# Performance work log

Measured on AMD Instinct MI355X. Metric: run time of the kernel, lower is better.

## Reference

```python
import jax, jax.numpy as jnp
import numpy as np

B, S, D, H = 2, 4096, 512, 8


def setup_inputs() -> dict:
    key = jax.random.key(0)
    ks = jax.random.split(key, 8)
    sc = 1.0 / np.sqrt(D)
    return {
        "query": jax.random.normal(ks[0], (B, S, D), jnp.float32),
        "key_in": jax.random.normal(ks[1], (B, S, D), jnp.float32),
        "value": jax.random.normal(ks[2], (B, S, D), jnp.float32),
        "mask": jax.random.randint(ks[3], (B, S), 0, 2, jnp.int32),
        "Wq": jax.random.normal(ks[4], (D, D), jnp.float32) * sc,
        "bq": jnp.zeros((D,), jnp.float32),
        "Wk": jax.random.normal(ks[5], (D, D), jnp.float32) * sc,
        "bk": jnp.zeros((D,), jnp.float32),
        "Wv": jax.random.normal(ks[6], (D, D), jnp.float32) * sc,
        "bv": jnp.zeros((D,), jnp.float32),
        "Wo": jax.random.normal(ks[7], (D, D), jnp.float32) * sc,
        "bo": jnp.zeros((D,), jnp.float32),
    }


def reference(query, key_in, value, mask, Wq, bq, Wk, bk, Wv, bv, Wo, bo):
    b, s, d = query.shape
    dh = d // H  # per-head dim = out_size // attn_heads
    # projections + split heads: [B,S,D] -> [B,H,S,dh]
    q = (query @ Wq + bq).reshape(b, s, H, dh).transpose(0, 2, 1, 3)
    k = (key_in @ Wk + bk).reshape(b, s, H, dh).transpose(0, 2, 1, 3)
    v = (value @ Wv + bv).reshape(b, s, H, dh).transpose(0, 2, 1, 3)
    # scores / sqrt(dh); torch divides by sqrt(query.size(-1)) AFTER head split
    scores = jnp.einsum("bhqd,bhkd->bhqk", q, k) / jnp.sqrt(jnp.asarray(dh, q.dtype))
    # 2D mask broadcast: mask[:,None,None,:] == unsqueeze(1).repeat(1,S,1).unsqueeze(1)
    scores = jnp.where(mask[:, None, None, :] == 0, jnp.asarray(-1e9, scores.dtype), scores)
    p_attn = jax.nn.softmax(scores, axis=-1)  # dropout p=0.0 -> identity
    x = jnp.einsum("bhqk,bhkd->bhqd", p_attn, v)
    x = x.transpose(0, 2, 1, 3).reshape(b, s, H * dh)
    return x @ Wo + bo
```

## Files before the change

### kernel.cpp

```cpp
#include <hip/hip_runtime.h>
#include <math.h>

#define BATCH  2
#define SLEN   4096
#define DMODEL 512
#define NH     8
#define DH     64
#define NROWS  (BATCH * SLEN)
#define NSPLIT 2
#define KSPLIT (SLEN / NSPLIT)

#define QSCALE 0.18033688011112042f
#define MBIAS  -65504.0f

typedef __attribute__((ext_vector_type(8)))  _Float16 f16x8;
typedef __attribute__((ext_vector_type(4)))  _Float16 f16x4;
typedef __attribute__((ext_vector_type(4)))  float    f32x4;
typedef __attribute__((ext_vector_type(16))) float    f32x16;
typedef __attribute__((ext_vector_type(4)))  unsigned int u32x4;

__device__ __forceinline__ float exp2_hw(float x) {
    float r; asm("v_exp_f32 %0, %1" : "=v"(r) : "v"(x)); return r;
}

__device__ __forceinline__ void pswap(unsigned &a, unsigned &b) {
    asm volatile("v_permlane32_swap_b32 %0, %1" : "+v"(a), "+v"(b));
}

__device__ __forceinline__ unsigned pkrtz(float a, float b) {
    auto p = __builtin_amdgcn_cvt_pkrtz(a, b);
    return __builtin_bit_cast(unsigned, p);
}

__device__ __forceinline__ void gload16(const void* g, void* l) {
    __builtin_amdgcn_global_load_lds(
        (const __attribute__((address_space(1))) unsigned int*)g,
        (__attribute__((address_space(3))) unsigned int*)l, 16, 0, 0);
}

__global__ __launch_bounds__(256)
void cast_weights(const float* __restrict__ W0, const float* __restrict__ W1,
                  const float* __restrict__ W2, const float* __restrict__ W3,
                  _Float16* __restrict__ T0, _Float16* __restrict__ T1,
                  _Float16* __restrict__ T2, _Float16* __restrict__ T3)
{
    const int z = blockIdx.z;
    const float* W = (z == 0) ? W0 : (z == 1) ? W1 : (z == 2) ? W2 : W3;
    _Float16*    T = (z == 0) ? T0 : (z == 1) ? T1 : (z == 2) ? T2 : T3;
    const float sc = (z == 0) ? QSCALE : 1.0f;

    __shared__ float Ls[32][33];
    const int n0 = blockIdx.x * 32, k0 = blockIdx.y * 32;
    const int row = threadIdx.x >> 3;
    const int c4  = (threadIdx.x & 7) << 2;

    float4 v = *(const float4*)&W[(size_t)(k0 + row) * DMODEL + n0 + c4];
    Ls[row][c4 + 0] = v.x; Ls[row][c4 + 1] = v.y;
    Ls[row][c4 + 2] = v.z; Ls[row][c4 + 3] = v.w;
    __syncthreads();

    f16x4 o;
    #pragma unroll
    for (int j = 0; j < 4; ++j) o[j] = (_Float16)(Ls[c4 + j][row] * sc);
    *(f16x4*)&T[(size_t)(n0 + row) * DMODEL + k0 + c4] = o;
}

template<int AMODE, int OUTMODE>
__global__ __launch_bounds__(256)
void gemm_mfma(const void* __restrict__ Ag, const _Float16* __restrict__ WTg,
               const float* __restrict__ bias, float bscale, void* __restrict__ Cout)
{
    extern __shared__ char smem[];
    char* Asb = smem;
    char* Bsb = smem + 8192;
    _Float16* Tr = (_Float16*)(smem + 16384);

    const int tid  = threadIdx.x;
    const int lane = tid & 63;
    const int w    = tid >> 6;
    const int g    = lane >> 4;
    const int c    = lane & 15;

    const int wg  = blockIdx.x;
    const int xcd = wg & 7;
    const int idx = wg >> 3;
    const int m0  = (xcd * 16 + (idx >> 3)) * 64;
    const int n0  = (idx & 7) * 64;

    const int lrow = lane >> 3;
    const int schk = (lane & 7) ^ lrow;
    const int brow = w * 8 + lrow;
    const _Float16* bSrc0 = WTg + (size_t)(n0 + brow) * DMODEL + schk * 8;
    const _Float16* bSrc1 = WTg + (size_t)(n0 + brow + 32) * DMODEL + schk * 8;
    char* bDst = Bsb + w * 1024;
    char* aDst = Asb + w * 1024;

    const _Float16* aSrc0 = nullptr; const _Float16* aSrc1 = nullptr;
    const float* aF = nullptr;
    const int arow = tid >> 2;
    const int acp  = (tid & 3) << 1;
    if constexpr (AMODE == 0) {
        const _Float16* Ah = (const _Float16*)Ag;
        aSrc0 = Ah + (size_t)(m0 + brow) * DMODEL + schk * 8;
        aSrc1 = Ah + (size_t)(m0 + brow + 32) * DMODEL + schk * 8;
    } else {
        aF = (const float*)Ag + (size_t)(m0 + arow) * DMODEL;
    }

    f32x4 acc[4];
    #pragma unroll
    for (int nt = 0; nt < 4; ++nt) acc[nt] = (f32x4){0.f, 0.f, 0.f, 0.f};

    for (int k0 = 0; k0 < DMODEL; k0 += 64) {
        float4 a0, a1, a2, a3;
        if constexpr (AMODE == 1) {
            const float* p = aF + k0 + acp * 8;
            a0 = *(const float4*)(p + 0);  a1 = *(const float4*)(p + 4);
            a2 = *(const float4*)(p + 8);  a3 = *(const float4*)(p + 12);
        }
        __syncthreads();
        if constexpr (AMODE == 0) {
            gload16(aSrc0 + k0, aDst);
            gload16(aSrc1 + k0, aDst + 4096);
        } else {
            f16x8 h0, h1;
            h0[0]=(_Float16)a0.x; h0[1]=(_Float16)a0.y; h0[2]=(_Float16)a0.z; h0[3]=(_Float16)a0.w;
            h0[4]=(_Float16)a1.x; h0[5]=(_Float16)a1.y; h0[6]=(_Float16)a1.z; h0[7]=(_Float16)a1.w;
            h1[0]=(_Float16)a2.x; h1[1]=(_Float16)a2.y; h1[2]=(_Float16)a2.z; h1[3]=(_Float16)a2.w;
            h1[4]=(_Float16)a3.x; h1[5]=(_Float16)a3.y; h1[6]=(_Float16)a3.z; h1[7]=(_Float16)a3.w;
            *(f16x8*)(Asb + arow * 128 + (((acp    ) ^ (arow & 7)) << 4)) = h0;
            *(f16x8*)(Asb + arow * 128 + (((acp + 1) ^ (arow & 7)) << 4)) = h1;
        }
        gload16(bSrc0 + k0, bDst);
        gload16(bSrc1 + k0, bDst + 4096);
        __syncthreads();

        #pragma unroll
        for (int ks = 0; ks < 2; ++ks) {
            const int ar = w * 16 + c;
            f16x8 af = *(const f16x8*)(Asb + ar * 128 + ((((ks << 2) + g) ^ (ar & 7)) << 4));
            #pragma unroll
            for (int nt = 0; nt < 4; ++nt) {
                const int br = nt * 16 + c;
                f16x8 bf = *(const f16x8*)(Bsb + br * 128 + ((((ks << 2) + g) ^ (br & 7)) << 4));
                acc[nt] = __builtin_amdgcn_mfma_f32_16x16x32_f16(af, bf, acc[nt], 0, 0, 0);
            }
        }
    }

    const int h = n0 >> 6;
    if constexpr (OUTMODE == 0) {
        float* C = (float*)Cout;
        #pragma unroll
        for (int nt = 0; nt < 4; ++nt) {
            const float bb = bias[n0 + nt * 16 + c];
            #pragma unroll
            for (int r = 0; r < 4; ++r) {
                const int m = m0 + w * 16 + g * 4 + r;
                C[(size_t)m * DMODEL + n0 + nt * 16 + c] = acc[nt][r] + bb;
            }
        }
    } else if constexpr (OUTMODE == 1) {
        _Float16* C = (_Float16*)Cout;
        #pragma unroll
        for (int nt = 0; nt < 4; ++nt) {
            const float bb = bias[n0 + nt * 16 + c] * bscale;
            const int hd = nt * 16 + c;
            #pragma unroll
            for (int r = 0; r < 4; ++r) {
                const int m = m0 + w * 16 + g * 4 + r;
                const int b = m >> 12;
                const int s = m & (SLEN - 1);
                C[(((size_t)b * NH + h) * SLEN + s) * DH + hd] = (_Float16)(acc[nt][r] + bb);
            }
        }
    } else {
        #pragma unroll
        for (int nt = 0; nt < 4; ++nt) {
            const float bb = bias[n0 + nt * 16 + c];
            #pragma unroll
            for (int r = 0; r < 4; ++r)
                Tr[(size_t)(w * 64 + nt * 16 + c) * 24 + g * 4 + r] = (_Float16)(acc[nt][r] + bb);
        }
        const int n = lane;
        f16x8 t0 = *(const f16x8*)&Tr[(size_t)(w * 64 + n) * 24 + 0];
        f16x8 t1 = *(const f16x8*)&Tr[(size_t)(w * 64 + n) * 24 + 8];
        const int b = m0 >> 12;
        const int s = (m0 & (SLEN - 1)) + w * 16;
        _Float16* dst = (_Float16*)Cout + (((size_t)b * NH + h) * DH + n) * SLEN + s;
        *(f16x8*)dst = t0;
        *(f16x8*)(dst + 8) = t1;
    }
}

__global__ __launch_bounds__(256, 4)
void flash_split(const _Float16* __restrict__ Qg, const _Float16* __restrict__ Kg,
                 const _Float16* __restrict__ Vtg, const int* __restrict__ mask,
                 _Float16* __restrict__ Op, float2* __restrict__ ML)
{
    __shared__ char KsB[8192];
    __shared__ char VsB[8192];
    __shared__ _Float16 Mb[64];
    __shared__ _Float16 Osc[4][32][72];

    const int tid  = threadIdx.x;
    const int lane = tid & 63;
    const int w    = tid >> 6;
    const int q    = lane & 31;
    const int h    = lane >> 5;

    const int wg    = blockIdx.x;
    const int xcd   = wg & 7;
    const int idx   = wg >> 3;
    const int combo = xcd * 4 + (idx >> 5);
    const int qt    = idx & 31;
    const int bh    = combo >> 1;
    const int sp    = combo & 1;
    const int b     = bh >> 3;
    const int q0    = qt * 128;
    const int kbase = sp * KSPLIT;

    const _Float16* Kb  = Kg  + (size_t)bh * SLEN * DH;
    const _Float16* Vtb = Vtg + (size_t)bh * DH * SLEN;
    const int* mrow = mask + (size_t)b * SLEN + kbase;

    const _Float16* Qb = Qg + ((size_t)bh * SLEN + q0 + w * 32 + q) * DH;
    f16x8 qf[4];
    #pragma unroll
    for (int ds = 0; ds < 4; ++ds) qf[ds] = *(const f16x8*)(Qb + ds * 16 + h * 8);

    f16x8 ef = (f16x8)(_Float16)0;
    if (h == 0) ef[0] = (_Float16)1;
    f16x8 onesA;
    #pragma unroll
    for (int i = 0; i < 8; ++i) onesA[i] = (_Float16)1;

    const int l8   = lane >> 3;
    const int schk = (lane & 7) ^ l8;
    const _Float16* kS0 = Kb  + (size_t)(kbase + w * 8 + l8) * DH + schk * 8;
    const _Float16* kS1 = kS0 + (size_t)32 * DH;
    const _Float16* vS0 = Vtb + (size_t)(w * 8 + l8) * SLEN + kbase + schk * 8;
    const _Float16* vS1 = vS0 + (size_t)32 * SLEN;
    char* kD0 = KsB + w * 1024;  char* kD1 = KsB + 4096 + w * 1024;
    char* vD0 = VsB + w * 1024;  char* vD1 = VsB + 4096 + w * 1024;

    float  mrun = -INFINITY;
    f32x16 lacc = (f32x16)0.f;
    f32x16 oacc[2];
    oacc[0] = (f32x16)0.f; oacc[1] = (f32x16)0.f;

    for (int kt = 0; kt < KSPLIT / 64; ++kt) {
        const int k0 = kt << 6;
        __syncthreads();
        gload16(kS0 + (size_t)k0 * DH, kD0);
        gload16(kS1 + (size_t)k0 * DH, kD1);
        gload16(vS0 + k0, vD0);
        gload16(vS1 + k0, vD1);
        if (tid < 64) Mb[tid] = mrow[k0 + tid] ? (_Float16)0 : (_Float16)MBIAS;
        __syncthreads();

        f32x16 st[2];
        #pragma unroll
        for (int kt2 = 0; kt2 < 2; ++kt2) {
            f16x8 mf = (f16x8)(_Float16)0;
            if (h == 0) mf[0] = Mb[q + kt2 * 32];
            st[kt2] = __builtin_amdgcn_mfma_f32_32x32x16_f16(mf, ef, (f32x16)0.f, 0, 0, 0);
            #pragma unroll
            for (int ds = 0; ds < 4; ++ds) {
                const int row = kt2 * 32 + q;
                f16x8 kf = *(const f16x8*)(KsB + row * 128 + ((((ds << 1) + h) ^ (row & 7)) << 4));
                st[kt2] = __builtin_amdgcn_mfma_f32_32x32x16_f16(kf, qf[ds], st[kt2], 0, 0, 0);
            }
        }

        float a[16];
        #pragma unroll
        for (int e = 0; e < 16; ++e) a[e] = fmaxf(st[0][e], st[1][e]);
        #pragma unroll
        for (int s2 = 8; s2 >= 1; s2 >>= 1) {
            #pragma unroll
            for (int e = 0; e < 8; ++e)
                if (e < s2) a[e] = fmaxf(a[e], a[e + s2]);
        }
        float mx = fmaxf(a[0], __shfl_xor(a[0], 32));
        const float mn   = fmaxf(mrun, mx);
        const float corr = exp2_hw(mrun - mn);
        mrun = mn;

        #pragma unroll
        for (int kt2 = 0; kt2 < 2; ++kt2) {
            #pragma unroll
            for (int e = 0; e < 16; ++e)
                st[kt2][e] = exp2_hw(st[kt2][e] - mn);
        }
        lacc[0] *= corr;
        #pragma unroll
        for (int e = 0; e < 16; ++e) { oacc[0][e] *= corr; oacc[1][e] *= corr; }

        #pragma unroll
        for (int ks = 0; ks < 4; ++ks) {
            const int kt2 = ks >> 1, bs = (ks & 1) * 8;
            unsigned W0 = pkrtz(st[kt2][bs + 0], st[kt2][bs + 1]);
            unsigned W1 = pkrtz(st[kt2][bs + 2], st[kt2][bs + 3]);
            unsigned W2 = pkrtz(st[kt2][bs + 4], st[kt2][bs + 5]);
            unsigned W3 = pkrtz(st[kt2][bs + 6], st[kt2][bs + 7]);
            pswap(W0, W2);
            pswap(W1, W3);
            u32x4 pw; pw[0] = W0; pw[1] = W1; pw[2] = W2; pw[3] = W3;
            f16x8 pb = __builtin_bit_cast(f16x8, pw);

            lacc = __builtin_amdgcn_mfma_f32_32x32x16_f16(onesA, pb, lacc, 0, 0, 0);
            #pragma unroll
            for (int dt = 0; dt < 2; ++dt) {
                const int row = dt * 32 + q;
                f16x8 vf = *(const f16x8*)(VsB + row * 128 + ((((ks << 1) + h) ^ (row & 7)) << 4));
                oacc[dt] = __builtin_amdgcn_mfma_f32_32x32x16_f16(vf, pb, oacc[dt], 0, 0, 0);
            }
        }
    }

    const float inv = 1.0f / lacc[0];
    #pragma unroll
    for (int dt = 0; dt < 2; ++dt) {
        #pragma unroll
        for (int r = 0; r < 16; r += 2) {
            const int d = dt * 32 + (r & 3) + 8 * (r >> 2) + 4 * h;
            *(unsigned*)&Osc[w][q][d] = pkrtz(oacc[dt][r] * inv, oacc[dt][r + 1] * inv);
        }
    }
    const size_t qabs = (size_t)(sp * 16 + bh) * SLEN + q0 + w * 32;
    if (h == 0) ML[qabs + q] = make_float2(mrun, lacc[0]);

    const int qr  = lane >> 1;
    const int dh2 = (lane & 1) * 32;
    _Float16* dst = Op + (qabs + qr) * DH + dh2;
    #pragma unroll
    for (int p = 0; p < 4; ++p)
        *(f16x8*)(dst + p * 8) = *(const f16x8*)&Osc[w][qr][dh2 + p * 8];
}

__global__ __launch_bounds__(256)
void combine_split(const _Float16* __restrict__ Op, const float2* __restrict__ ML,
                   _Float16* __restrict__ X)
{
    const int bh = blockIdx.x >> 7;
    const int qb = blockIdx.x & 127;
    const int q  = qb * 32 + (threadIdx.x >> 3);
    const int dc = (threadIdx.x & 7) * 8;

    const size_t i1 = (size_t)bh * SLEN + q;
    const size_t i2 = (size_t)(16 + bh) * SLEN + q;
    const float2 ml1 = ML[i1];
    const float2 ml2 = ML[i2];
    const float m  = fmaxf(ml1.x, ml2.x);
    const float a1 = exp2_hw(ml1.x - m) * ml1.y;
    const float a2 = exp2_hw(ml2.x - m) * ml2.y;
    const float w1 = a1 / (a1 + a2);
    const float w2 = 1.0f - w1;

    f16x8 o1 = *(const f16x8*)(Op + i1 * DH + dc);
    f16x8 o2 = *(const f16x8*)(Op + i2 * DH + dc);
    f16x8 o;
    #pragma unroll
    for (int j = 0; j < 8; ++j)
        o[j] = (_Float16)(w1 * (float)o1[j] + w2 * (float)o2[j]);

    const int b  = bh >> 3;
    const int hh = bh & 7;
    *(f16x8*)(X + ((size_t)b * SLEN + q) * DMODEL + hh * DH + dc) = o;
}

extern "C" void kernel_launch(void* const* d_in, const int* in_sizes, int n_in,
                              void* d_out, int out_size, void* d_ws, size_t ws_size,
                              hipStream_t stream)
{
    const float* query  = (const float*)d_in[0];
    const float* key_in = (const float*)d_in[1];
    const float* value  = (const float*)d_in[2];
    const int*   mask   = (const int*)  d_in[3];
    const float* Wq = (const float*)d_in[4];
    const float* bq = (const float*)d_in[5];
    const float* Wk = (const float*)d_in[6];
    const float* bk = (const float*)d_in[7];
    const float* Wv = (const float*)d_in[8];
    const float* bv = (const float*)d_in[9];
    const float* Wo = (const float*)d_in[10];
    const float* bo = (const float*)d_in[11];
    float* out = (float*)d_out;
    (void)in_sizes; (void)n_in; (void)out_size; (void)ws_size;

    const size_t NE = (size_t)NROWS * DMODEL;
    const size_t WN = (size_t)DMODEL * DMODEL;
    const size_t OPN = (size_t)NSPLIT * NH * BATCH * SLEN * DH;
    _Float16* f   = (_Float16*)d_ws;
    _Float16* qh  = f;
    _Float16* kh  = f + NE;
    _Float16* vth = f + 2 * NE;
    _Float16* xh  = f + 3 * NE;
    _Float16* wqT = f + 4 * NE;
    _Float16* wkT = wqT + WN;
    _Float16* wvT = wkT + WN;
    _Float16* woT = wvT + WN;
    _Float16* opart = woT + WN;
    float2*   mlpart = (float2*)(opart + OPN);

    cast_weights<<<dim3(16, 16, 4), 256, 0, stream>>>(Wq, Wk, Wv, Wo, wqT, wkT, wvT, woT);

    gemm_mfma<1, 1><<<1024, 256, 16384, stream>>>(query,  wqT, bq, QSCALE, qh);
    gemm_mfma<1, 1><<<1024, 256, 16384, stream>>>(key_in, wkT, bk, 1.0f,   kh);
    gemm_mfma<1, 2><<<1024, 256, 28672, stream>>>(value,  wvT, bv, 1.0f,   vth);

    flash_split<<<1024, 256, 0, stream>>>(qh, kh, vth, mask, opart, mlpart);
    combine_split<<<2048, 256, 0, stream>>>(opart, mlpart, xh);

    gemm_mfma<0, 0><<<1024, 256, 16384, stream>>>(xh, woT, bo, 1.0f, out);
}
```

Before: 173.3 us.

## Merge QKV projections into one launch, double-buffer flash tiles, lazy max rescale

The three input projection GEMMs become one 3072-block launch that picks Q/K/V by block index, and the output projection gets its own specialized kernel. The flash attention kernel double-buffers K/V and mask tiles in shared memory, so the next tile's loads are issued before the current tile is computed. Its occupancy hint drops from 4 to 3. The online softmax now rescales only when the tile max grows by more than a threshold, and folds the running-max subtraction into the mask MFMA via an fp16 bias. This removes per-tile correction work but relies on fp16 rounding of the max and a bounded exponent growth.

```diff
diff --git a/kernel.cpp b/kernel.cpp
--- a/kernel.cpp
+++ b/kernel.cpp
@@ -9,6 +9,7 @@
 #define NROWS  (BATCH * SLEN)
 #define NSPLIT 2
 #define KSPLIT (SLEN / NSPLIT)
+#define NT     (KSPLIT / 64)
 
 #define QSCALE 0.18033688011112042f
 #define MBIAS  -65504.0f
@@ -65,15 +66,26 @@
     *(f16x4*)&T[(size_t)(n0 + row) * DMODEL + k0 + c4] = o;
 }
 
-template<int AMODE, int OUTMODE>
 __global__ __launch_bounds__(256)
-void gemm_mfma(const void* __restrict__ Ag, const _Float16* __restrict__ WTg,
-               const float* __restrict__ bias, float bscale, void* __restrict__ Cout)
+void gemm_qkv(const float* __restrict__ Aq, const float* __restrict__ Ak,
+              const float* __restrict__ Av,
+              const _Float16* __restrict__ Wqt, const _Float16* __restrict__ Wkt,
+              const _Float16* __restrict__ Wvt,
+              const float* __restrict__ bqp, const float* __restrict__ bkp,
+              const float* __restrict__ bvp,
+              _Float16* __restrict__ Cq, _Float16* __restrict__ Ck,
+              _Float16* __restrict__ Cv)
 {
     extern __shared__ char smem[];
     char* Asb = smem;
     char* Bsb = smem + 8192;
     _Float16* Tr = (_Float16*)(smem + 16384);
+
+    const int z  = blockIdx.x >> 10;
+    const int wg = blockIdx.x & 1023;
+    const float*     A    = (z == 0) ? Aq  : (z == 1) ? Ak  : Av;
+    const _Float16*  WTg  = (z == 0) ? Wqt : (z == 1) ? Wkt : Wvt;
+    const float*     bias = (z == 0) ? bqp : (z == 1) ? bkp : bvp;
 
     const int tid  = threadIdx.x;
     const int lane = tid & 63;
@@ -81,7 +93,6 @@
     const int g    = lane >> 4;
     const int c    = lane & 15;
 
-    const int wg  = blockIdx.x;
     const int xcd = wg & 7;
     const int idx = wg >> 3;
     const int m0  = (xcd * 16 + (idx >> 3)) * 64;
@@ -93,44 +104,27 @@
     const _Float16* bSrc0 = WTg + (size_t)(n0 + brow) * DMODEL + schk * 8;
     const _Float16* bSrc1 = WTg + (size_t)(n0 + brow + 32) * DMODEL + schk * 8;
     char* bDst = Bsb + w * 1024;
-    char* aDst = Asb + w * 1024;
-
-    const _Float16* aSrc0 = nullptr; const _Float16* aSrc1 = nullptr;
-    const float* aF = nullptr;
+
     const int arow = tid >> 2;
     const int acp  = (tid & 3) << 1;
-    if constexpr (AMODE == 0) {
-        const _Float16* Ah = (const _Float16*)Ag;
-        aSrc0 = Ah + (size_t)(m0 + brow) * DMODEL + schk * 8;
-        aSrc1 = Ah + (size_t)(m0 + brow + 32) * DMODEL + schk * 8;
-    } else {
-        aF = (const float*)Ag + (size_t)(m0 + arow) * DMODEL;
-    }
+    const float* aF = A + (size_t)(m0 + arow) * DMODEL;
 
     f32x4 acc[4];
     #pragma unroll
     for (int nt = 0; nt < 4; ++nt) acc[nt] = (f32x4){0.f, 0.f, 0.f, 0.f};
 
     for (int k0 = 0; k0 < DMODEL; k0 += 64) {
-        float4 a0, a1, a2, a3;
-        if constexpr (AMODE == 1) {
-            const float* p = aF + k0 + acp * 8;
-            a0 = *(const float4*)(p + 0);  a1 = *(const float4*)(p + 4);
-            a2 = *(const float4*)(p + 8);  a3 = *(const float4*)(p + 12);
-        }
+        const float* p = aF + k0 + acp * 8;
+        float4 a0 = *(const float4*)(p + 0);  float4 a1 = *(const float4*)(p + 4);
+        float4 a2 = *(const float4*)(p + 8);  float4 a3 = *(const float4*)(p + 12);
         __syncthreads();
-        if constexpr (AMODE == 0) {
-            gload16(aSrc0 + k0, aDst);
-            gload16(aSrc1 + k0, aDst + 4096);
-        } else {
-            f16x8 h0, h1;
-            h0[0]=(_Float16)a0.x; h0[1]=(_Float16)a0.y; h0[2]=(_Float16)a0.z; h0[3]=(_Float16)a0.w;
-            h0[4]=(_Float16)a1.x; h0[5]=(_Float16)a1.y; h0[6]=(_Float16)a1.z; h0[7]=(_Float16)a1.w;
-            h1[0]=(_Float16)a2.x; h1[1]=(_Float16)a2.y; h1[2]=(_Float16)a2.z; h1[3]=(_Float16)a2.w;
-            h1[4]=(_Float16)a3.x; h1[5]=(_Float16)a3.y; h1[6]=(_Float16)a3.z; h1[7]=(_Float16)a3.w;
-            *(f16x8*)(Asb + arow * 128 + (((acp    ) ^ (arow & 7)) << 4)) = h0;
-            *(f16x8*)(Asb + arow * 128 + (((acp + 1) ^ (arow & 7)) << 4)) = h1;
-        }
+        f16x8 h0, h1;
+        h0[0]=(_Float16)a0.x; h0[1]=(_Float16)a0.y; h0[2]=(_Float16)a0.z; h0[3]=(_Float16)a0.w;
+        h0[4]=(_Float16)a1.x; h0[5]=(_Float16)a1.y; h0[6]=(_Float16)a1.z; h0[7]=(_Float16)a1.w;
+        h1[0]=(_Float16)a2.x; h1[1]=(_Float16)a2.y; h1[2]=(_Float16)a2.z; h1[3]=(_Float16)a2.w;
+        h1[4]=(_Float16)a3.x; h1[5]=(_Float16)a3.y; h1[6]=(_Float16)a3.z; h1[7]=(_Float16)a3.w;
+        *(f16x8*)(Asb + arow * 128 + (((acp    ) ^ (arow & 7)) << 4)) = h0;
+        *(f16x8*)(Asb + arow * 128 + (((acp + 1) ^ (arow & 7)) << 4)) = h1;
         gload16(bSrc0 + k0, bDst);
         gload16(bSrc1 + k0, bDst + 4096);
         __syncthreads();
@@ -149,22 +143,12 @@
     }
 
     const int h = n0 >> 6;
-    if constexpr (OUTMODE == 0) {
-        float* C = (float*)Cout;
+    if (z < 2) {
+        _Float16* C = z ? Ck : Cq;
+        const float bsc = z ? 1.0f : QSCALE;
         #pragma unroll
         for (int nt = 0; nt < 4; ++nt) {
-            const float bb = bias[n0 + nt * 16 + c];
-            #pragma unroll
-            for (int r = 0; r < 4; ++r) {
-                const int m = m0 + w * 16 + g * 4 + r;
-                C[(size_t)m * DMODEL + n0 + nt * 16 + c] = acc[nt][r] + bb;
-            }
-        }
-    } else if constexpr (OUTMODE == 1) {
-        _Float16* C = (_Float16*)Cout;
-        #pragma unroll
-        for (int nt = 0; nt < 4; ++nt) {
-            const float bb = bias[n0 + nt * 16 + c] * bscale;
+            const float bb = bias[n0 + nt * 16 + c] * bsc;
             const int hd = nt * 16 + c;
             #pragma unroll
             for (int r = 0; r < 4; ++r) {
@@ -187,20 +171,84 @@
         f16x8 t1 = *(const f16x8*)&Tr[(size_t)(w * 64 + n) * 24 + 8];
         const int b = m0 >> 12;
         const int s = (m0 & (SLEN - 1)) + w * 16;
-        _Float16* dst = (_Float16*)Cout + (((size_t)b * NH + h) * DH + n) * SLEN + s;
+        _Float16* dst = Cv + (((size_t)b * NH + h) * DH + n) * SLEN + s;
         *(f16x8*)dst = t0;
         *(f16x8*)(dst + 8) = t1;
     }
 }
 
-__global__ __launch_bounds__(256, 4)
+__global__ __launch_bounds__(256)
+void gemm_out(const _Float16* __restrict__ Ah, const _Float16* __restrict__ WTg,
+              const float* __restrict__ bias, float* __restrict__ Cout)
+{
+    __shared__ char Asb[8192];
+    __shared__ char Bsb[8192];
+
+    const int tid  = threadIdx.x;
+    const int lane = tid & 63;
+    const int w    = tid >> 6;
+    const int g    = lane >> 4;
+    const int c    = lane & 15;
+
+    const int wg  = blockIdx.x;
+    const int xcd = wg & 7;
+    const int idx = wg >> 3;
+    const int m0  = (xcd * 16 + (idx >> 3)) * 64;
+    const int n0  = (idx & 7) * 64;
+
+    const int lrow = lane >> 3;
+    const int schk = (lane & 7) ^ lrow;
+    const int brow = w * 8 + lrow;
+    const _Float16* bSrc0 = WTg + (size_t)(n0 + brow) * DMODEL + schk * 8;
+    const _Float16* bSrc1 = WTg + (size_t)(n0 + brow + 32) * DMODEL + schk * 8;
+    const _Float16* aSrc0 = Ah + (size_t)(m0 + brow) * DMODEL + schk * 8;
+    const _Float16* aSrc1 = Ah + (size_t)(m0 + brow + 32) * DMODEL + schk * 8;
+    char* bDst = Bsb + w * 1024;
+    char* aDst = Asb + w * 1024;
+
+    f32x4 acc[4];
+    #pragma unroll
+    for (int nt = 0; nt < 4; ++nt) acc[nt] = (f32x4){0.f, 0.f, 0.f, 0.f};
+
+    for (int k0 = 0; k0 < DMODEL; k0 += 64) {
+        __syncthreads();
+        gload16(aSrc0 + k0, aDst);
+        gload16(aSrc1 + k0, aDst + 4096);
+        gload16(bSrc0 + k0, bDst);
+        gload16(bSrc1 + k0, bDst + 4096);
+        __syncthreads();
+
+        #pragma unroll
+        for (int ks = 0; ks < 2; ++ks) {
+            const int ar = w * 16 + c;
+            f16x8 af = *(const f16x8*)(Asb + ar * 128 + ((((ks << 2) + g) ^ (ar & 7)) << 4));
+            #pragma unroll
+            for (int nt = 0; nt < 4; ++nt) {
+                const int br = nt * 16 + c;
+                f16x8 bf = *(const f16x8*)(Bsb + br * 128 + ((((ks << 2) + g) ^ (br & 7)) << 4));
+                acc[nt] = __builtin_amdgcn_mfma_f32_16x16x32_f16(af, bf, acc[nt], 0, 0, 0);
+            }
+        }
+    }
+
+    #pragma unroll
+    for (int nt = 0; nt < 4; ++nt) {
+        const float bb = bias[n0 + nt * 16 + c];
+        #pragma unroll
+        for (int r = 0; r < 4; ++r) {
+            const int m = m0 + w * 16 + g * 4 + r;
+            Cout[(size_t)m * DMODEL + n0 + nt * 16 + c] = acc[nt][r] + bb;
+        }
+    }
+}
+
+__global__ __launch_bounds__(256, 3)
 void flash_split(const _Float16* __restrict__ Qg, const _Float16* __restrict__ Kg,
                  const _Float16* __restrict__ Vtg, const int* __restrict__ mask,
                  _Float16* __restrict__ Op, float2* __restrict__ ML)
 {
-    __shared__ char KsB[8192];
-    __shared__ char VsB[8192];
-    __shared__ _Float16 Mb[64];
+    __shared__ char SB[2][16384];
+    __shared__ _Float16 Mb2[2][64];
     __shared__ _Float16 Osc[4][32][72];
 
     const int tid  = threadIdx.x;
@@ -229,8 +277,6 @@
     #pragma unroll
     for (int ds = 0; ds < 4; ++ds) qf[ds] = *(const f16x8*)(Qb + ds * 16 + h * 8);
 
-    f16x8 ef = (f16x8)(_Float16)0;
-    if (h == 0) ef[0] = (_Float16)1;
     f16x8 onesA;
     #pragma unroll
     for (int i = 0; i < 8; ++i) onesA[i] = (_Float16)1;
@@ -241,30 +287,50 @@
     const _Float16* kS1 = kS0 + (size_t)32 * DH;
     const _Float16* vS0 = Vtb + (size_t)(w * 8 + l8) * SLEN + kbase + schk * 8;
     const _Float16* vS1 = vS0 + (size_t)32 * SLEN;
-    char* kD0 = KsB + w * 1024;  char* kD1 = KsB + 4096 + w * 1024;
-    char* vD0 = VsB + w * 1024;  char* vD1 = VsB + 4096 + w * 1024;
-
-    float  mrun = -INFINITY;
+
+    float  mrun = 0.0f;
+    _Float16 nmr = (_Float16)0.0f;
     f32x16 lacc = (f32x16)0.f;
     f32x16 oacc[2];
     oacc[0] = (f32x16)0.f; oacc[1] = (f32x16)0.f;
 
-    for (int kt = 0; kt < KSPLIT / 64; ++kt) {
-        const int k0 = kt << 6;
+    {
+        char* d = (char*)SB[0] + w * 1024;
+        gload16(kS0, d);
+        gload16(kS1, d + 4096);
+        gload16(vS0, d + 8192);
+        gload16(vS1, d + 12288);
+        if (tid < 64) Mb2[0][tid] = mrow[tid] ? (_Float16)0 : (_Float16)MBIAS;
+    }
+
+    int cur = 0;
+    for (int kt = 0; kt < NT; ++kt) {
         __syncthreads();
-        gload16(kS0 + (size_t)k0 * DH, kD0);
-        gload16(kS1 + (size_t)k0 * DH, kD1);
-        gload16(vS0 + k0, vD0);
-        gload16(vS1 + k0, vD1);
-        if (tid < 64) Mb[tid] = mrow[k0 + tid] ? (_Float16)0 : (_Float16)MBIAS;
-        __syncthreads();
+        if (kt + 1 < NT) {
+            const int k0n = (kt + 1) << 6;
+            char* d = (char*)SB[cur ^ 1] + w * 1024;
+            gload16(kS0 + (size_t)k0n * DH, d);
+            gload16(kS1 + (size_t)k0n * DH, d + 4096);
+            gload16(vS0 + k0n, d + 8192);
+            gload16(vS1 + k0n, d + 12288);
+            if (tid < 64)
+                Mb2[cur ^ 1][tid] = mrow[k0n + tid] ? (_Float16)0 : (_Float16)MBIAS;
+        }
+        const char* KsB = (const char*)SB[cur];
+        const char* VsB = KsB + 8192;
 
         f32x16 st[2];
         #pragma unroll
         for (int kt2 = 0; kt2 < 2; ++kt2) {
             f16x8 mf = (f16x8)(_Float16)0;
-            if (h == 0) mf[0] = Mb[q + kt2 * 32];
-            st[kt2] = __builtin_amdgcn_mfma_f32_32x32x16_f16(mf, ef, (f32x16)0.f, 0, 0, 0);
+            f16x8 ev = (f16x8)(_Float16)0;
+            if (h == 0) {
+                mf[0] = Mb2[cur][q + kt2 * 32];
+                mf[1] = (_Float16)1;
+                ev[0] = (_Float16)1;
+                ev[1] = nmr;
+            }
+            st[kt2] = __builtin_amdgcn_mfma_f32_32x32x16_f16(mf, ev, (f32x16)0.f, 0, 0, 0);
             #pragma unroll
             for (int ds = 0; ds < 4; ++ds) {
                 const int row = kt2 * 32 + q;
@@ -283,19 +349,32 @@
                 if (e < s2) a[e] = fmaxf(a[e], a[e + s2]);
         }
         float mx = fmaxf(a[0], __shfl_xor(a[0], 32));
-        const float mn   = fmaxf(mrun, mx);
-        const float corr = exp2_hw(mrun - mn);
-        mrun = mn;
-
-        #pragma unroll
-        for (int kt2 = 0; kt2 < 2; ++kt2) {
-            #pragma unroll
-            for (int e = 0; e < 16; ++e)
-                st[kt2][e] = exp2_hw(st[kt2][e] - mn);
-        }
-        lacc[0] *= corr;
-        #pragma unroll
-        for (int e = 0; e < 16; ++e) { oacc[0][e] *= corr; oacc[1][e] *= corr; }
+
+        if (__builtin_expect(!__all(mx <= 8.0f), 0)) {
+            const float cand = mrun + mx;
+            const _Float16 mh = (_Float16)cand;
+            const float mn16 = (float)mh;
+            const float delta = mn16 - mrun;
+            const float corr  = exp2_hw(-delta);
+            mrun = mn16;
+            nmr  = (_Float16)(-mrun);
+            lacc[0] *= corr;
+            #pragma unroll
+            for (int e = 0; e < 16; ++e) { oacc[0][e] *= corr; oacc[1][e] *= corr; }
+            #pragma unroll
+            for (int kt2 = 0; kt2 < 2; ++kt2) {
+                #pragma unroll
+                for (int e = 0; e < 16; ++e)
+                    st[kt2][e] = exp2_hw(st[kt2][e] - delta);
+            }
+        } else {
+            #pragma unroll
+            for (int kt2 = 0; kt2 < 2; ++kt2) {
+                #pragma unroll
+                for (int e = 0; e < 16; ++e)
+                    st[kt2][e] = exp2_hw(st[kt2][e]);
+            }
+        }
 
         #pragma unroll
         for (int ks = 0; ks < 4; ++ks) {
@@ -317,6 +396,7 @@
                 oacc[dt] = __builtin_amdgcn_mfma_f32_32x32x16_f16(vf, pb, oacc[dt], 0, 0, 0);
             }
         }
+        cur ^= 1;
     }
 
     const float inv = 1.0f / lacc[0];
@@ -406,12 +486,12 @@
 
     cast_weights<<<dim3(16, 16, 4), 256, 0, stream>>>(Wq, Wk, Wv, Wo, wqT, wkT, wvT, woT);
 
-    gemm_mfma<1, 1><<<1024, 256, 16384, stream>>>(query,  wqT, bq, QSCALE, qh);
-    gemm_mfma<1, 1><<<1024, 256, 16384, stream>>>(key_in, wkT, bk, 1.0f,   kh);
-    gemm_mfma<1, 2><<<1024, 256, 28672, stream>>>(value,  wvT, bv, 1.0f,   vth);
+    gemm_qkv<<<3072, 256, 28672, stream>>>(query, key_in, value,
+                                           wqT, wkT, wvT, bq, bk, bv,
+                                           qh, kh, vth);
 
     flash_split<<<1024, 256, 0, stream>>>(qh, kh, vth, mask, opart, mlpart);
     combine_split<<<2048, 256, 0, stream>>>(opart, mlpart, xh);
 
-    gemm_mfma<0, 0><<<1024, 256, 16384, stream>>>(xh, woT, bo, 1.0f, out);
-}
+    gemm_out<<<1024, 256, 0, stream>>>(xh, woT, bo, out);
+}
```

After: 314.1 us. 81.3% more time.
